# Performance work log

Measured on AMD Instinct MI355X. Metric: run time of the kernel, lower is better.

Reference implementation:

```python
import jax, jax.numpy as jnp
import numpy as np
import math

IN_FEATURES = 4096
OUT_FEATURES = 4096
TOKENS = 8192


def hydrate_weight(seed, out_features, in_features):
    """Deterministically synthesize the virtual weight matrix from the 64-bit seed.
    Mirrors nn.Linear's kaiming-uniform-style bound (1/sqrt(fan_in)) used by gmem_rs
    hydration; never stored as a parameter."""
    bound = 1.0 / math.sqrt(in_features)
    key = jax.random.key(seed)
    return jax.random.uniform(
        key, (out_features, in_features), dtype=jnp.float32,
        minval=-bound, maxval=bound)


def setup_inputs() -> dict:
    key = jax.random.key(0)
    kx, kb = jax.random.split(key)
    x = jax.random.normal(kx, (TOKENS, IN_FEATURES), dtype=jnp.float32)
    bound = 1.0 / math.sqrt(IN_FEATURES)
    bias = jax.random.uniform(kb, (OUT_FEATURES,), dtype=jnp.float32,
                              minval=-bound, maxval=bound)
    return {"x": x, "bias": bias, "seed": 1140071481}


def reference(x, bias, seed):
    # Hydrate weight on-the-fly from seed (zero-RAM virtual weight), then GEMM.
    W = hydrate_weight(seed, OUT_FEATURES, IN_FEATURES)  # [out, in]
    y = jnp.einsum('ti,oi->to', x, W)  # [tokens, out]
    return y + bias
```

## Files before the change

### kernel.cpp

```cpp
#include <hip/hip_runtime.h>
#include <hip/hip_bf16.h>
#include <stdint.h>

#define TOKENS 8192
#define NOUT   4096
#define KIN    4096

#define BM 256
#define BN 256
#define BK 64
#define NT (KIN / BK)

typedef __attribute__((ext_vector_type(8))) short bf16x8;
typedef __attribute__((ext_vector_type(4))) float f32x4;

__device__ __forceinline__ uint32_t rotl32(uint32_t x, int r) {
  return (x << r) | (x >> (32 - r));
}

__device__ __forceinline__ uint16_t f2bf_rne(float f) {
  uint32_t u = __float_as_uint(f);
  u += 0x7FFFu + ((u >> 16) & 1u);
  return (uint16_t)(u >> 16);
}

__device__ __forceinline__ void threefry2x32(uint32_t k0, uint32_t k1,
                                             uint32_t c0, uint32_t c1,
                                             uint32_t& o0, uint32_t& o1) {
  uint32_t ks2 = 0x1BD11BDAu ^ k0 ^ k1;
  uint32_t x0 = c0 + k0;
  uint32_t x1 = c1 + k1;
#define TFR(r) { x0 += x1; x1 = rotl32(x1, (r)); x1 ^= x0; }
  TFR(13) TFR(15) TFR(26) TFR(6)
  x0 += k1;  x1 += ks2 + 1u;
  TFR(17) TFR(29) TFR(16) TFR(24)
  x0 += ks2; x1 += k0 + 2u;
  TFR(13) TFR(15) TFR(26) TFR(6)
  x0 += k0;  x1 += k1 + 3u;
  TFR(17) TFR(29) TFR(16) TFR(24)
  x0 += k1;  x1 += ks2 + 4u;
  TFR(13) TFR(15) TFR(26) TFR(6)
  x0 += ks2; x1 += k0 + 5u;
#undef TFR
  o0 = x0; o1 = x1;
}

__global__ void prep_kernel(const float* __restrict__ x,
                            uint16_t* __restrict__ xb,
                            uint16_t* __restrict__ W,
                            const int* __restrict__ seed_ptr) {
  uint32_t b = blockIdx.x;
  uint32_t g = b / 5u, r = b % 5u;
  if (r < 4u) {
    uint32_t k1 = (uint32_t)(*seed_ptr);
    uint32_t j = (g * 4u + r) * 256u + threadIdx.x;
    uint32_t o0, o1;
    threefry2x32(0u, k1, 0u, j, o0, o1);
    uint32_t bits = o0 ^ o1;
    const float scale = 0.03125f;
    const float mn    = -0.015625f;
    float f = __uint_as_float((bits >> 9) | 0x3F800000u) - 1.0f;
    float v = fmaxf(mn, f * scale + mn);
    W[j] = f2bf_rne(v);
  } else {
    uint32_t base = (g * 256u + threadIdx.x) * 8u;
    f32x4 a = *(const f32x4*)(x + base);
    f32x4 c = *(const f32x4*)(x + base + 4);
    union { uint16_t u[8]; bf16x8 v; } rr;
    rr.u[0] = f2bf_rne(a[0]); rr.u[1] = f2bf_rne(a[1]);
    rr.u[2] = f2bf_rne(a[2]); rr.u[3] = f2bf_rne(a[3]);
    rr.u[4] = f2bf_rne(c[0]); rr.u[5] = f2bf_rne(c[1]);
    rr.u[6] = f2bf_rne(c[2]); rr.u[7] = f2bf_rne(c[3]);
    *(bf16x8*)(xb + base) = rr.v;
  }
}

__global__ __launch_bounds__(512, 2)
void gemm_bias_kernel(const uint16_t* __restrict__ A,
                      const uint16_t* __restrict__ B,
                      const float* __restrict__ bias,
                      float* __restrict__ C) {
  __shared__ uint16_t smem[2][2][16384];

  const int nwgn = NOUT / BN;
  const int nwg  = (TOKENS / BM) * nwgn;
  int bid = blockIdx.x;
  int cpx = nwg >> 3;
  int swzb = (bid & 7) * cpx + (bid >> 3);
  const int tm = (swzb / nwgn) * BM;
  const int tn = (swzb % nwgn) * BN;

  const int t    = threadIdx.x;
  const int lane = t & 63;
  const int wid  = t >> 6;
  const int wm   = wid >> 2;
  const int wn   = wid & 3;
  const int fr   = lane & 15;
  const int fq   = lane >> 4;

  const int swzRd = (lane & 7) << 4;
  const int lsw   = ((lane & 7) ^ (lane >> 3)) << 4;

  const char* sA  = (const char*)(A + (size_t)(tm + wid * 16 + (lane >> 3)) * KIN) + lsw;
  const char* sB  = (const char*)(B + (size_t)(tn + wid * 16 + (lane >> 3)) * KIN) + lsw;
  const char* sA1 = sA + (size_t)128 * KIN * 2;
  const char* sB1 = sB + (size_t)128 * KIN * 2;

  char* const smemB = (char*)&smem[0][0][0];
  char* const dstB  = smemB + wid * 2048 + lane * 16;

  const int rA00 = (wm * 64 + fr) * 128 + ((fq << 4) ^ swzRd);
  const int rA01 = rA00 ^ 64;
  const int rA10 = rA00 + 65536;
  const int rA11 = rA10 ^ 64;
  const int rB00 = 32768 + (wn * 32 + fr) * 128 + ((fq << 4) ^ swzRd);
  const int rB01 = rB00 ^ 64;
  const int rB10 = rB00 + 65536;
  const int rB11 = rB10 ^ 64;

  f32x4 acc[8][4] = {};
  bf16x8 af[2][4], bv0[2][2], bv1[2][2];

  auto stage2 = [&](const char* src, char* dst) {
    __builtin_amdgcn_global_load_lds(
        (const __attribute__((address_space(1))) void*)src,
        (__attribute__((address_space(3))) void*)dst, 16, 0, 0);
    __builtin_amdgcn_global_load_lds(
        (const __attribute__((address_space(1))) void*)(src + (size_t)8 * KIN * 2),
        (__attribute__((address_space(3))) void*)(dst + 1024), 16, 0, 0);
  };

#define VMW(N) asm volatile("s_waitcnt vmcnt(" #N ")" ::: "memory")
#define LKW(N) asm volatile("s_waitcnt lgkmcnt(" #N ")" ::: "memory")
#define SB0    __builtin_amdgcn_sched_barrier(0)
#define PRI(p) __builtin_amdgcn_s_setprio(p)

#define RD_A4(BASE, S)                                                         \
    _Pragma("unroll")                                                          \
    for (int i_ = 0; i_ < 4; ++i_)                                             \
      af[S][i_] = *(const bf16x8*)(smemB + (BASE) + i_ * 2048);

#define RD_B2(BASE, BV, S)                                                     \
    _Pragma("unroll")                                                          \
    for (int j_ = 0; j_ < 2; ++j_)                                             \
      BV[S][j_] = *(const bf16x8*)(smemB + (BASE) + j_ * 2048);

#define MF8(MH, NH, BV, S)                                                     \
    _Pragma("unroll")                                                          \
    for (int i_ = 0; i_ < 4; ++i_)                                             \
      _Pragma("unroll")                                                        \
      for (int j_ = 0; j_ < 2; ++j_)                                           \
        acc[(MH) * 4 + i_][(NH) * 2 + j_] =                                    \
            __builtin_amdgcn_mfma_f32_16x16x32_bf16(                           \
                af[S][i_], BV[S][j_], acc[(MH) * 4 + i_][(NH) * 2 + j_],       \
                0, 0, 0);

#define KTILE(BUF, OFF1, OFF2, MODE)                                           \
  {                                                                            \
                       \
    RD_A4((BUF) ? rA10 : rA00, 0) RD_B2((BUF) ? rB10 : rB00, bv0, 0)           \
    SB0;                                                                       \
    RD_A4((BUF) ? rA11 : rA01, 1) RD_B2((BUF) ? rB11 : rB01, bv0, 1)           \
    if ((MODE) <= 1) stage2(sA1 + (OFF1),                                      \
                            dstB + ((BUF) ^ 1) * 65536 + 16384);               \
    __builtin_amdgcn_s_barrier();                                              \
    LKW(6); SB0; PRI(1); MF8(0, 0, bv0, 0)                                     \
    LKW(0); SB0; MF8(0, 0, bv0, 1) PRI(0);                                     \
                                                   \
    RD_B2(((BUF) ? rB10 : rB00) + 16384, bv1, 0)                               \
    SB0;                                                                       \
    RD_B2(((BUF) ? rB11 : rB01) + 16384, bv1, 1)                               \
    __builtin_amdgcn_s_barrier();                                              \
    LKW(2); SB0; PRI(1); MF8(0, 1, bv1, 0)                                     \
    LKW(0); SB0; MF8(0, 1, bv1, 1) PRI(0);                                     \
            \
    RD_A4(((BUF) ? rA10 : rA00) + 16384, 0)                                    \
    SB0;                                                                       \
    RD_A4(((BUF) ? rA11 : rA01) + 16384, 1)                                    \
    if ((MODE) == 0) { stage2(sA + (OFF2), dstB + (BUF) * 65536);              \
                       stage2(sB + (OFF2), dstB + (BUF) * 65536 + 32768); }    \
    __builtin_amdgcn_s_barrier();                                              \
    LKW(4); SB0; PRI(1); MF8(1, 1, bv1, 0)                                     \
    LKW(0); SB0; MF8(1, 1, bv1, 1) PRI(0);                                     \
        \
    if ((MODE) == 0) stage2(sB1 + (OFF2), dstB + (BUF) * 65536 + 49152);       \
    if ((MODE) == 0) { VMW(6); } else if ((MODE) == 1) { VMW(0); }             \
    __builtin_amdgcn_s_barrier();                                              \
    SB0; PRI(1); MF8(1, 0, bv0, 0) MF8(1, 0, bv0, 1) PRI(0);                   \
  }

  stage2(sA,        dstB);
  stage2(sB,        dstB + 32768);
  stage2(sA1,       dstB + 16384);
  stage2(sB1,       dstB + 49152);
  stage2(sA  + 128, dstB + 65536);
  stage2(sB  + 128, dstB + 65536 + 32768);
  stage2(sB1 + 128, dstB + 65536 + 49152);
  VMW(6);
  __builtin_amdgcn_s_barrier();

  for (int it = 0; it < (NT - 2) / 2; ++it) {
    KTILE(0, 128, 256, 0)
    KTILE(1, 256, 384, 0)
    sA += 256; sB += 256; sA1 += 256; sB1 += 256;
  }
  KTILE(0, 128, 0, 1)
  KTILE(1, 0, 0, 2)

#undef KTILE
#undef MF8
#undef RD_B2
#undef RD_A4
#undef PRI
#undef SB0
#undef LKW
#undef VMW

#pragma unroll
  for (int nj = 0; nj < 4; ++nj) {
    const int nh = nj >> 1, j = nj & 1;
    const int col = tn + wn * 32 + nh * 128 + j * 16 + fr;
    const float bvs = bias[col];
#pragma unroll
    for (int mi = 0; mi < 8; ++mi) {
      const int mh = mi >> 2, i = mi & 3;
      const int row0 = tm + wm * 64 + mh * 128 + i * 16 + fq * 4;
#pragma unroll
      for (int rr = 0; rr < 4; ++rr)
        C[(size_t)(row0 + rr) * NOUT + col] = acc[mi][nj][rr] + bvs;
    }
  }
}

extern "C" void kernel_launch(void* const* d_in, const int* in_sizes, int n_in,
                              void* d_out, int out_size, void* d_ws, size_t ws_size,
                              hipStream_t stream) {
  const float* x    = (const float*)d_in[0];
  const float* bias = (const float*)d_in[1];
  const int*   seed = (const int*)d_in[2];
  float* y = (float*)d_out;

  uint16_t* Wb = (uint16_t*)d_ws;
  uint16_t* Xb = Wb + (size_t)NOUT * KIN;

  prep_kernel<<<81920, 256, 0, stream>>>(x, Xb, Wb, seed);

  const int grid = (TOKENS / BM) * (NOUT / BN);
  gemm_bias_kernel<<<grid, 512, 0, stream>>>(Xb, Wb, bias, y);
}
```

Baseline: 251.1 us.

## Halve GEMM K-tile to 32 with reworked LDS swizzle and finer MFMA interleave

Reduces the K tile from 64 to 32, halving LDS usage per buffer (64KB instead of 128KB total). Staging becomes one global_load_lds per thread per quarter-tile, and the LDS swizzle and read offsets are redone for 64-byte rows. MFMA groups are split into smaller batches interleaved with LDS reads. The aim is lower LDS pressure and possibly more occupancy or finer overlap, at the cost of twice as many barriers and loop iterations per K.

Measured after the change: 259.0 us. 3.2% more time.

```diff
diff --git a/kernel.cpp b/kernel.cpp
--- a/kernel.cpp
+++ b/kernel.cpp
@@ -8,7 +8,7 @@
 
 #define BM 256
 #define BN 256
-#define BK 64
+#define BK 32
 #define NT (KIN / BK)
 
 typedef __attribute__((ext_vector_type(8))) short bf16x8;
@@ -80,7 +80,7 @@
                       const uint16_t* __restrict__ B,
                       const float* __restrict__ bias,
                       float* __restrict__ C) {
-  __shared__ uint16_t smem[2][2][16384];
+  __shared__ uint16_t smem[2][2][8192];
 
   const int nwgn = NOUT / BN;
   const int nwg  = (TOKENS / BM) * nwgn;
@@ -98,36 +98,27 @@
   const int fr   = lane & 15;
   const int fq   = lane >> 4;
 
-  const int swzRd = (lane & 7) << 4;
-  const int lsw   = ((lane & 7) ^ (lane >> 3)) << 4;
-
-  const char* sA  = (const char*)(A + (size_t)(tm + wid * 16 + (lane >> 3)) * KIN) + lsw;
-  const char* sB  = (const char*)(B + (size_t)(tn + wid * 16 + (lane >> 3)) * KIN) + lsw;
+  const int swzRd = ((fr >> 1) & 3) << 4;
+  const int lsw   = (((lane & 3) ^ ((lane >> 3) & 3))) << 4;
+
+  const char* sA  = (const char*)(A + (size_t)(tm + wid * 16 + (lane >> 2)) * KIN) + lsw;
+  const char* sB  = (const char*)(B + (size_t)(tn + wid * 16 + (lane >> 2)) * KIN) + lsw;
   const char* sA1 = sA + (size_t)128 * KIN * 2;
   const char* sB1 = sB + (size_t)128 * KIN * 2;
 
   char* const smemB = (char*)&smem[0][0][0];
-  char* const dstB  = smemB + wid * 2048 + lane * 16;
-
-  const int rA00 = (wm * 64 + fr) * 128 + ((fq << 4) ^ swzRd);
-  const int rA01 = rA00 ^ 64;
-  const int rA10 = rA00 + 65536;
-  const int rA11 = rA10 ^ 64;
-  const int rB00 = 32768 + (wn * 32 + fr) * 128 + ((fq << 4) ^ swzRd);
-  const int rB01 = rB00 ^ 64;
-  const int rB10 = rB00 + 65536;
-  const int rB11 = rB10 ^ 64;
+  char* const dstB  = smemB + wid * 1024 + lane * 16;
+
+  const int rA0 = (wm * 64 + fr) * 64 + ((fq << 4) ^ swzRd);
+  const int rB0 = 16384 + (wn * 32 + fr) * 64 + ((fq << 4) ^ swzRd);
 
   f32x4 acc[8][4] = {};
-  bf16x8 af[2][4], bv0[2][2], bv1[2][2];
-
-  auto stage2 = [&](const char* src, char* dst) {
+  bf16x8 af[4], bv0[2], bv1[2];
+
+  auto stage1 = [&](const char* src, char* dst) {
     __builtin_amdgcn_global_load_lds(
         (const __attribute__((address_space(1))) void*)src,
         (__attribute__((address_space(3))) void*)dst, 16, 0, 0);
-    __builtin_amdgcn_global_load_lds(
-        (const __attribute__((address_space(1))) void*)(src + (size_t)8 * KIN * 2),
-        (__attribute__((address_space(3))) void*)(dst + 1024), 16, 0, 0);
   };
 
 #define VMW(N) asm volatile("s_waitcnt vmcnt(" #N ")" ::: "memory")
@@ -135,82 +126,87 @@
 #define SB0    __builtin_amdgcn_sched_barrier(0)
 #define PRI(p) __builtin_amdgcn_s_setprio(p)
 
-#define RD_A4(BASE, S)                                                         \
-    _Pragma("unroll")                                                          \
-    for (int i_ = 0; i_ < 4; ++i_)                                             \
-      af[S][i_] = *(const bf16x8*)(smemB + (BASE) + i_ * 2048);
-
-#define RD_B2(BASE, BV, S)                                                     \
-    _Pragma("unroll")                                                          \
-    for (int j_ = 0; j_ < 2; ++j_)                                             \
-      BV[S][j_] = *(const bf16x8*)(smemB + (BASE) + j_ * 2048);
-
-#define MF8(MH, NH, BV, S)                                                     \
-    _Pragma("unroll")                                                          \
-    for (int i_ = 0; i_ < 4; ++i_)                                             \
-      _Pragma("unroll")                                                        \
-      for (int j_ = 0; j_ < 2; ++j_)                                           \
-        acc[(MH) * 4 + i_][(NH) * 2 + j_] =                                    \
-            __builtin_amdgcn_mfma_f32_16x16x32_bf16(                           \
-                af[S][i_], BV[S][j_], acc[(MH) * 4 + i_][(NH) * 2 + j_],       \
-                0, 0, 0);
+#define MF1(MH, NH, I, J, BV)                                                  \
+    acc[(MH) * 4 + (I)][(NH) * 2 + (J)] =                                      \
+        __builtin_amdgcn_mfma_f32_16x16x32_bf16(                               \
+            af[I], BV[J], acc[(MH) * 4 + (I)][(NH) * 2 + (J)], 0, 0, 0);
+
+#define MF_I01(MH, NH, BV) MF1(MH, NH, 0, 0, BV) MF1(MH, NH, 0, 1, BV)         \
+                           MF1(MH, NH, 1, 0, BV) MF1(MH, NH, 1, 1, BV)
+#define MF_I23(MH, NH, BV) MF1(MH, NH, 2, 0, BV) MF1(MH, NH, 2, 1, BV)         \
+                           MF1(MH, NH, 3, 0, BV) MF1(MH, NH, 3, 1, BV)
+#define MF_J0(MH, NH, BV)  MF1(MH, NH, 0, 0, BV) MF1(MH, NH, 1, 0, BV)         \
+                           MF1(MH, NH, 2, 0, BV) MF1(MH, NH, 3, 0, BV)
+#define MF_J1(MH, NH, BV)  MF1(MH, NH, 0, 1, BV) MF1(MH, NH, 1, 1, BV)         \
+                           MF1(MH, NH, 2, 1, BV) MF1(MH, NH, 3, 1, BV)
+#define MF_ALL(MH, NH, BV) MF_I01(MH, NH, BV) MF_I23(MH, NH, BV)
 
 #define KTILE(BUF, OFF1, OFF2, MODE)                                           \
   {                                                                            \
-                       \
-    RD_A4((BUF) ? rA10 : rA00, 0) RD_B2((BUF) ? rB10 : rB00, bv0, 0)           \
+    const int aB = rA0 + (BUF) * 32768;                                        \
+    const int bB = rB0 + (BUF) * 32768;                                        \
+            \
+    af[0] = *(const bf16x8*)(smemB + aB);                                      \
+    af[1] = *(const bf16x8*)(smemB + aB + 1024);                               \
+    bv0[0] = *(const bf16x8*)(smemB + bB);                                     \
+    bv0[1] = *(const bf16x8*)(smemB + bB + 1024);                              \
     SB0;                                                                       \
-    RD_A4((BUF) ? rA11 : rA01, 1) RD_B2((BUF) ? rB11 : rB01, bv0, 1)           \
-    if ((MODE) <= 1) stage2(sA1 + (OFF1),                                      \
-                            dstB + ((BUF) ^ 1) * 65536 + 16384);               \
-    __builtin_amdgcn_s_barrier();                                              \
-    LKW(6); SB0; PRI(1); MF8(0, 0, bv0, 0)                                     \
-    LKW(0); SB0; MF8(0, 0, bv0, 1) PRI(0);                                     \
-                                                   \
-    RD_B2(((BUF) ? rB10 : rB00) + 16384, bv1, 0)                               \
+    af[2] = *(const bf16x8*)(smemB + aB + 2048);                               \
+    af[3] = *(const bf16x8*)(smemB + aB + 3072);                               \
+    if ((MODE) <= 1) stage1(sA1 + (OFF1), dstB + ((BUF) ^ 1) * 32768 + 8192);  \
+    __builtin_amdgcn_s_barrier();                                              \
+    LKW(2); SB0; PRI(1); MF_I01(0, 0, bv0)                                     \
+    LKW(0); SB0; MF_I23(0, 0, bv0) PRI(0);                                     \
+                         \
+    bv1[0] = *(const bf16x8*)(smemB + bB + 8192);                              \
     SB0;                                                                       \
-    RD_B2(((BUF) ? rB11 : rB01) + 16384, bv1, 1)                               \
-    __builtin_amdgcn_s_barrier();                                              \
-    LKW(2); SB0; PRI(1); MF8(0, 1, bv1, 0)                                     \
-    LKW(0); SB0; MF8(0, 1, bv1, 1) PRI(0);                                     \
-            \
-    RD_A4(((BUF) ? rA10 : rA00) + 16384, 0)                                    \
+    bv1[1] = *(const bf16x8*)(smemB + bB + 8192 + 1024);                       \
+    if ((MODE) == 0) stage1(sA + (OFF2), dstB + (BUF) * 32768);                \
+    __builtin_amdgcn_s_barrier();                                              \
+    LKW(1); SB0; PRI(1); MF_J0(0, 1, bv1)                                      \
+    LKW(0); SB0; MF_J1(0, 1, bv1) PRI(0);                                      \
+              \
+    af[0] = *(const bf16x8*)(smemB + aB + 8192);                               \
+    af[1] = *(const bf16x8*)(smemB + aB + 8192 + 1024);                        \
     SB0;                                                                       \
-    RD_A4(((BUF) ? rA11 : rA01) + 16384, 1)                                    \
-    if ((MODE) == 0) { stage2(sA + (OFF2), dstB + (BUF) * 65536);              \
-                       stage2(sB + (OFF2), dstB + (BUF) * 65536 + 32768); }    \
-    __builtin_amdgcn_s_barrier();                                              \
-    LKW(4); SB0; PRI(1); MF8(1, 1, bv1, 0)                                     \
-    LKW(0); SB0; MF8(1, 1, bv1, 1) PRI(0);                                     \
-        \
-    if ((MODE) == 0) stage2(sB1 + (OFF2), dstB + (BUF) * 65536 + 49152);       \
-    if ((MODE) == 0) { VMW(6); } else if ((MODE) == 1) { VMW(0); }             \
-    __builtin_amdgcn_s_barrier();                                              \
-    SB0; PRI(1); MF8(1, 0, bv0, 0) MF8(1, 0, bv0, 1) PRI(0);                   \
-  }
-
-  stage2(sA,        dstB);
-  stage2(sB,        dstB + 32768);
-  stage2(sA1,       dstB + 16384);
-  stage2(sB1,       dstB + 49152);
-  stage2(sA  + 128, dstB + 65536);
-  stage2(sB  + 128, dstB + 65536 + 32768);
-  stage2(sB1 + 128, dstB + 65536 + 49152);
-  VMW(6);
+    af[2] = *(const bf16x8*)(smemB + aB + 8192 + 2048);                        \
+    af[3] = *(const bf16x8*)(smemB + aB + 8192 + 3072);                        \
+    if ((MODE) == 0) stage1(sB + (OFF2), dstB + (BUF) * 32768 + 16384);        \
+    __builtin_amdgcn_s_barrier();                                              \
+    LKW(2); SB0; PRI(1); MF_I01(1, 1, bv1)                                     \
+    LKW(0); SB0; MF_I23(1, 1, bv1) PRI(0);                                     \
+         \
+    if ((MODE) == 0) stage1(sB1 + (OFF2), dstB + (BUF) * 32768 + 24576);       \
+    if ((MODE) == 0) { VMW(3); } else if ((MODE) == 1) { VMW(0); }             \
+    __builtin_amdgcn_s_barrier();                                              \
+    SB0; PRI(1); MF_ALL(1, 0, bv0) PRI(0);                                     \
+  }
+
+  stage1(sA,        dstB);
+  stage1(sB,        dstB + 16384);
+  stage1(sA1,       dstB + 8192);
+  stage1(sB1,       dstB + 24576);
+  stage1(sA  + 64,  dstB + 32768);
+  stage1(sB  + 64,  dstB + 32768 + 16384);
+  stage1(sB1 + 64,  dstB + 32768 + 24576);
+  VMW(3);
   __builtin_amdgcn_s_barrier();
 
   for (int it = 0; it < (NT - 2) / 2; ++it) {
-    KTILE(0, 128, 256, 0)
-    KTILE(1, 256, 384, 0)
-    sA += 256; sB += 256; sA1 += 256; sB1 += 256;
-  }
-  KTILE(0, 128, 0, 1)
+    KTILE(0, 64, 128, 0)
+    KTILE(1, 128, 192, 0)
+    sA += 128; sB += 128; sA1 += 128; sB1 += 128;
+  }
+  KTILE(0, 64, 0, 1)
   KTILE(1, 0, 0, 2)
 
 #undef KTILE
-#undef MF8
-#undef RD_B2
-#undef RD_A4
+#undef MF_ALL
+#undef MF_J1
+#undef MF_J0
+#undef MF_I23
+#undef MF_I01
+#undef MF1
 #undef PRI
 #undef SB0
 #undef LKW
```
